# Performance work log

Hardware: AMD Instinct MI355X
Metric: run time of the kernel (lower is better)

## Reference

```python
import jax, jax.numpy as jnp
import numpy as np

N_HEAD = 8
NORM_GROUPS = 32
EPS = 1e-6


def setup_inputs() -> dict:
    key = jax.random.key(0)
    ks = jax.random.split(key, 9)
    B, C, H, W, D = 1, 256, 16, 16, 16
    COND = 512
    x = jax.random.normal(ks[0], (B, C, H, W, D), dtype=jnp.float32)
    cond = jax.random.normal(ks[1], (B, COND), dtype=jnp.float32)
    # AdaGN linear scale/shift (torch Linear: weight [C, cond_dim], bias [C])
    w_scale = jax.random.normal(ks[2], (C, COND), dtype=jnp.float32) * 0.02
    b_scale = jax.random.normal(ks[3], (C,), dtype=jnp.float32) * 0.02
    w_shift = jax.random.normal(ks[4], (C, COND), dtype=jnp.float32) * 0.02
    b_shift = jax.random.normal(ks[5], (C,), dtype=jnp.float32) * 0.02
    # 1x1x1 conv3d weights collapse to matrices: qkv [3C, C] (no bias), out [C, C] + bias
    w_qkv = jax.random.normal(ks[6], (3 * C, C), dtype=jnp.float32) * (1.0 / np.sqrt(C))
    w_out = jax.random.normal(ks[7], (C, C), dtype=jnp.float32) * (1.0 / np.sqrt(C))
    b_out = jax.random.normal(ks[8], (C,), dtype=jnp.float32) * 0.02
    return {"x": x, "cond": cond, "w_scale": w_scale, "b_scale": b_scale,
            "w_shift": w_shift, "b_shift": b_shift, "w_qkv": w_qkv,
            "w_out": w_out, "b_out": b_out}


def _ada_gn(x, cond, w_scale, b_scale, w_shift, b_shift):
    B, C, H, W, D = x.shape
    G = NORM_GROUPS
    xg = x.reshape(B, G, C // G, H, W, D)
    mean = jnp.mean(xg, axis=(2, 3, 4, 5), keepdims=True)
    var = jnp.var(xg, axis=(2, 3, 4, 5), keepdims=True)
    x_norm = ((xg - mean) * jax.lax.rsqrt(var + EPS)).reshape(B, C, H, W, D)
    scale = (cond @ w_scale.T + b_scale)[:, :, None, None, None]  # [B,C,1,1,1]
    shift = (cond @ w_shift.T + b_shift)[:, :, None, None, None]
    return x_norm * (1.0 + scale) + shift


def reference(x, cond, w_scale, b_scale, w_shift, b_shift, w_qkv, w_out, b_out):
    B, C, H, W, D = x.shape
    nh = N_HEAD
    hd = C // nh
    N = H * W * D  # flattened spatial tokens
    norm = _ada_gn(x, cond, w_scale, b_scale, w_shift, b_shift)
    # 1x1x1 conv == channel matmul
    qkv = jnp.einsum('oc,bchwd->bohwd', w_qkv, norm)        # [B,3C,H,W,D]
    qkv = qkv.reshape(B, nh, 3 * hd, N)
    q, k, v = jnp.split(qkv, 3, axis=2)                      # each [B,nh,hd,N]
    attn = jnp.einsum('bnci,bncj->bnij', q, k) / jnp.sqrt(jnp.float32(C))
    attn = jax.nn.softmax(attn, axis=-1)                     # [B,nh,N,N]
    out = jnp.einsum('bnij,bncj->bnci', attn, v)             # [B,nh,hd,N]
    out = out.reshape(B, C, H, W, D)
    out = jnp.einsum('oc,bchwd->bohwd', w_out, out) + b_out[None, :, None, None, None]
    return out + x
```

## Files before the change

kernel.cpp:

```cpp
#include <hip/hip_runtime.h>
#include <math.h>

#define CCH 256
#define NN  4096
#define NHEAD 8
#define CONDD 512

typedef __attribute__((ext_vector_type(8))) short short8;
typedef __attribute__((ext_vector_type(4))) float f32x4;
typedef __attribute__((ext_vector_type(16))) float f32x16;

static __device__ __forceinline__ short f2bf(float f) {
    union { float f; uint32_t u; } v; v.f = f;
    uint32_t r = v.u + 0x7fffu + ((v.u >> 16) & 1u);
    return (short)(r >> 16);
}

static __device__ __forceinline__ uint32_t cvt_pk_bf16(float a, float b) {
    uint32_t r;
    asm("v_cvt_pk_bf16_f32 %0, %1, %2" : "=v"(r) : "v"(a), "v"(b));
    return r;
}

__global__ __launch_bounds__(256) void front_fused(const float* __restrict__ x,
                                                   const float* __restrict__ cond,
                                                   const float* __restrict__ w_scale,
                                                   const float* __restrict__ b_scale,
                                                   const float* __restrict__ w_shift,
                                                   const float* __restrict__ b_shift,
                                                   const float* __restrict__ wq,
                                                   const float* __restrict__ wo,
                                                   float* __restrict__ partial,
                                                   float* __restrict__ scale,
                                                   float* __restrict__ shift,
                                                   short* __restrict__ wqb,
                                                   short* __restrict__ wob) {
    __shared__ float rs[4], rss[4];
    int bb = blockIdx.x;
    int t = threadIdx.x;
    if (bb < 256) {
        const float4* p = (const float4*)(x + bb * 4096);
        float s = 0.f, ss = 0.f;
        for (int k = t; k < 1024; k += 256) {
            float4 v = p[k];
            s += v.x + v.y + v.z + v.w;
            ss += v.x * v.x + v.y * v.y + v.z * v.z + v.w * v.w;
        }
        #pragma unroll
        for (int off = 32; off; off >>= 1) { s += __shfl_xor(s, off); ss += __shfl_xor(ss, off); }
        int wid = t >> 6;
        if ((t & 63) == 0) { rs[wid] = s; rss[wid] = ss; }
        __syncthreads();
        if (t == 0) {
            partial[2 * bb] = rs[0] + rs[1] + rs[2] + rs[3];
            partial[2 * bb + 1] = rss[0] + rss[1] + rss[2] + rss[3];
        }
    } else if (bb < 1280) {
        int idx = (bb - 256) * 256 + t;
        if (idx < 196608) wqb[idx] = f2bf(wq[idx]);
        else              wob[idx - 196608] = f2bf(wo[idx - 196608]);
    } else {
        int o = (bb - 1280) * 4 + (t >> 6);
        int lane = t & 63;
        float ds = 0.f, dh = 0.f;
        for (int k = lane; k < CONDD; k += 64) {
            float cv = cond[k];
            ds += cv * w_scale[o * CONDD + k];
            dh += cv * w_shift[o * CONDD + k];
        }
        #pragma unroll
        for (int off = 32; off; off >>= 1) { ds += __shfl_xor(ds, off); dh += __shfl_xor(dh, off); }
        if (lane == 0) { scale[o] = ds + b_scale[o]; shift[o] = dh + b_shift[o]; }
    }
}

__global__ __launch_bounds__(256) void normalize_t(const float* __restrict__ x,
                                                   const float* __restrict__ partial,
                                                   const float* __restrict__ scale,
                                                   const float* __restrict__ shift,
                                                   short* __restrict__ norm_t) {
    __shared__ float gm[8], gr[8];
    __shared__ float Aa[64], Bb[64];
    __shared__ short tile[32 * 66];
    int i0 = blockIdx.x * 32;
    int c0 = blockIdx.y * 64;
    int g0 = c0 >> 3;
    int t = threadIdx.x;
    if (t < 8) {
        float s = 0.f, ss = 0.f;
        #pragma unroll
        for (int ch = 0; ch < 8; ++ch) {
            s += partial[((g0 + t) * 8 + ch) * 2];
            ss += partial[((g0 + t) * 8 + ch) * 2 + 1];
        }
        float mean = s * (1.0f / 32768.0f);
        float var = ss * (1.0f / 32768.0f) - mean * mean;
        gm[t] = mean;
        gr[t] = rsqrtf(var + 1e-6f);
    }
    __syncthreads();
    if (t < 64) {
        int c = c0 + t;
        float a = gr[t >> 3] * (1.0f + scale[c]);
        Aa[t] = a;
        Bb[t] = shift[c] - gm[t >> 3] * a;
    }
    __syncthreads();
    #pragma unroll
    for (int e0 = 0; e0 < 8; ++e0) {
        int e = e0 * 256 + t;
        int cl = e >> 5, il = e & 31;
        float v = x[(c0 + cl) * NN + i0 + il];
        tile[il * 66 + cl] = f2bf(v * Aa[cl] + Bb[cl]);
    }
    __syncthreads();
    #pragma unroll
    for (int e0 = 0; e0 < 4; ++e0) {
        int e = e0 * 256 + t;
        int il = e >> 5, cd = e & 31;
        uint32_t d = *(const uint32_t*)&tile[il * 66 + 2 * cd];
        *(uint32_t*)&norm_t[(i0 + il) * 256 + c0 + 2 * cd] = d;
    }
}

__global__ __launch_bounds__(256) void qkv_gemm(const short* __restrict__ wqb,
                                                const short* __restrict__ norm_t,
                                                short* __restrict__ qtb, short* __restrict__ ktb,
                                                short* __restrict__ vcb) {
    int t = threadIdx.x;
    int w = t >> 6, lane = t & 63, li = lane & 15, lg = lane >> 4;
    int o0 = blockIdx.x * 32;
    int i0 = blockIdx.y * 64 + w * 16;
    f32x4 acc[2] = {{0,0,0,0},{0,0,0,0}};
    const short* bbase = norm_t + (i0 + li) * 256 + 8 * lg;
    const short* abase = wqb + (o0 + li) * 256 + 8 * lg;
    #pragma unroll
    for (int ks = 0; ks < 8; ++ks) {
        short8 bfrag = *(const short8*)(bbase + ks * 32);
        #pragma unroll
        for (int f = 0; f < 2; ++f) {
            short8 afrag = *(const short8*)(abase + f * 16 * 256 + ks * 32);
            acc[f] = __builtin_amdgcn_mfma_f32_16x16x32_bf16(afrag, bfrag, acc[f], 0, 0, 0);
        }
    }
    int i = i0 + li;
    #pragma unroll
    for (int f = 0; f < 2; ++f) {
        #pragma unroll
        for (int r = 0; r < 4; ++r) {
            int o = o0 + 16 * f + 4 * lg + r;
            float v = acc[f][r];
            int h = o / 96;
            int rr = o - h * 96;
            int cc = rr & 31;
            int kind = rr >> 5;
            if (kind == 0)      qtb[(h * NN + i) * 32 + cc] = f2bf(v * (0.0625f * 1.44269504f));
            else if (kind == 1) ktb[(h * NN + i) * 32 + cc] = f2bf(v);
            else                vcb[(h * 32 + cc) * NN + i] = f2bf(v);
        }
    }
}

__global__ __launch_bounds__(256, 4) void attention_mfma(const short* __restrict__ qtb,
                                                         const short* __restrict__ ktb,
                                                         const short* __restrict__ vcb,
                                                         float* __restrict__ pacc,
                                                         float* __restrict__ plsum) {
    __shared__ __align__(16) short kbuf[2][2048];
    __shared__ __align__(16) short vbuf[2][2048];

    int bid = blockIdx.x;
    int h = bid & 7;
    int qb = (bid >> 3) & 31;
    int kh = bid >> 8;
    int t = threadIdx.x;
    int w = t >> 6, lane = t & 63, l31 = lane & 31, hi = lane >> 5;

    int qbase = qb * 128 + w * 32;
    const short* qrow = qtb + (h * NN + qbase + l31) * 32;
    short8 qf0 = *(const short8*)(qrow + 8 * hi);
    short8 qf1 = *(const short8*)(qrow + 16 + 8 * hi);

    int kr_ = t >> 2, ks_ = t & 3, kg_ = ks_ ^ (kr_ & 3);
    int vr_ = t >> 3, vs_ = t & 7, vg_ = vs_ ^ (vr_ & 7);
    const char* kgbase = (const char*)(ktb + (h * NN + kh * 2048) * 32) + kr_ * 64 + kg_ * 16;
    const char* vgbase = (const char*)(vcb + (h * 32 + vr_) * NN + kh * 2048) + vg_ * 16;
    int wave_off = (t >> 6) * 1024;

    f32x16 acc = {0,0,0,0,0,0,0,0,0,0,0,0,0,0,0,0};
    const f32x16 zero16 = {0,0,0,0,0,0,0,0,0,0,0,0,0,0,0,0};
    float lsum = 0.f;

    __builtin_amdgcn_global_load_lds((const uint32_t*)kgbase, (uint32_t*)((char*)&kbuf[0][0] + wave_off), 16, 0, 0);
    __builtin_amdgcn_global_load_lds((const uint32_t*)vgbase, (uint32_t*)((char*)&vbuf[0][0] + wave_off), 16, 0, 0);
    __syncthreads();

    #pragma unroll 1
    for (int st = 0; st < 32; ++st) {
        int cur = st & 1;
        if (st < 31) {
            const char* kn = kgbase + (st + 1) * 4096;
            const char* vn = vgbase + (st + 1) * 128;
            __builtin_amdgcn_global_load_lds((const uint32_t*)kn, (uint32_t*)((char*)&kbuf[cur ^ 1][0] + wave_off), 16, 0, 0);
            __builtin_amdgcn_global_load_lds((const uint32_t*)vn, (uint32_t*)((char*)&vbuf[cur ^ 1][0] + wave_off), 16, 0, 0);
        }

        #pragma unroll
        for (int half = 0; half < 2; ++half) {
            int jl = half * 32;
            int R = jl + l31;
            const short* kr = &kbuf[cur][R * 32];
            int rx = R & 3;
            short8 kf0 = *(const short8*)(kr + ((hi ^ rx) << 3));
            short8 kf1 = *(const short8*)(kr + (((2 + hi) ^ rx) << 3));
            const short* vr = &vbuf[cur][l31 * 64];
            int cx = l31 & 7;
            int s0 = (jl >> 3) + hi;
            short8 vf0 = *(const short8*)(vr + ((s0 ^ cx) << 3));
            short8 vf1 = *(const short8*)(vr + (((s0 + 2) ^ cx) << 3));

            __builtin_amdgcn_s_setprio(1);
            f32x16 s = __builtin_amdgcn_mfma_f32_32x32x16_bf16(kf0, qf0, zero16, 0, 0, 0);
            s = __builtin_amdgcn_mfma_f32_32x32x16_bf16(kf1, qf1, s, 0, 0, 0);
            __builtin_amdgcn_s_setprio(0);

            float p[16];
            #pragma unroll
            for (int r = 0; r < 16; ++r) p[r] = __builtin_amdgcn_exp2f(s[r]);

            float u0 = 0.f, u1 = 0.f;
            #pragma unroll
            for (int r = 0; r < 4; ++r) { u0 += p[r] + p[4 + r]; u1 += p[8 + r] + p[12 + r]; }
            lsum += u0 + u1;

            auto A1 = __builtin_amdgcn_permlane32_swap(cvt_pk_bf16(p[0], p[1]),   cvt_pk_bf16(p[4], p[5]),   false, false);
            auto A2 = __builtin_amdgcn_permlane32_swap(cvt_pk_bf16(p[2], p[3]),   cvt_pk_bf16(p[6], p[7]),   false, false);
            auto A3 = __builtin_amdgcn_permlane32_swap(cvt_pk_bf16(p[8], p[9]),   cvt_pk_bf16(p[12], p[13]), false, false);
            auto A4 = __builtin_amdgcn_permlane32_swap(cvt_pk_bf16(p[10], p[11]), cvt_pk_bf16(p[14], p[15]), false, false);

            union PF { uint32_t u[4]; short8 s8; };
            PF f1, f2;
            f1.u[0] = A1[0]; f1.u[1] = A2[0]; f1.u[2] = A1[1]; f1.u[3] = A2[1];
            f2.u[0] = A3[0]; f2.u[1] = A4[0]; f2.u[2] = A3[1]; f2.u[3] = A4[1];

            __builtin_amdgcn_s_setprio(1);
            acc = __builtin_amdgcn_mfma_f32_32x32x16_bf16(vf0, f1.s8, acc, 0, 0, 0);
            acc = __builtin_amdgcn_mfma_f32_32x32x16_bf16(vf1, f2.s8, acc, 0, 0, 0);
            __builtin_amdgcn_s_setprio(0);
        }
        __syncthreads();
    }

    lsum += __shfl_xor(lsum, 32);

    int qg = qbase + l31;
    float* pb = pacc + ((kh * 8 + h) * 32) * NN + qg;
    #pragma unroll
    for (int r = 0; r < 16; ++r) {
        int c = (r & 3) + 8 * (r >> 2) + 4 * hi;
        pb[c * NN] = acc[r];
    }
    if (hi == 0) plsum[(kh * 8 + h) * NN + qg] = lsum;
}

__global__ __launch_bounds__(256) void attn_merge(const float* __restrict__ pacc,
                                                  const float* __restrict__ plsum,
                                                  short* __restrict__ attnT) {
    __shared__ float tile[64][33];
    __shared__ float invl[64];
    int it = blockIdx.x;
    int h = blockIdx.y;
    int t = threadIdx.x;
    int i0 = it * 64;
    int c = t >> 3, ic = (t & 7) * 8;
    const float* p0 = pacc + (h * 32 + c) * NN + i0 + ic;
    const float* p1 = pacc + ((8 + h) * 32 + c) * NN + i0 + ic;
    #pragma unroll
    for (int k = 0; k < 8; ++k) tile[ic + k][c] = p0[k] + p1[k];
    if (t < 64) {
        float ls = plsum[h * NN + i0 + t] + plsum[(8 + h) * NN + i0 + t];
        invl[t] = 1.0f / ls;
    }
    __syncthreads();
    int i = t >> 2, cs = (t & 3) * 8;
    float iv = invl[i];
    const float* tr = &tile[i][cs];
    uint4 o;
    o.x = cvt_pk_bf16(tr[0] * iv, tr[1] * iv);
    o.y = cvt_pk_bf16(tr[2] * iv, tr[3] * iv);
    o.z = cvt_pk_bf16(tr[4] * iv, tr[5] * iv);
    o.w = cvt_pk_bf16(tr[6] * iv, tr[7] * iv);
    *(uint4*)&attnT[(i0 + i) * 256 + h * 32 + cs] = o;
}

__global__ __launch_bounds__(256) void proj_gemm(const short* __restrict__ wob,
                                                 const short* __restrict__ attnT,
                                                 const float* __restrict__ b_out,
                                                 const float* __restrict__ x,
                                                 float* __restrict__ out) {
    int t = threadIdx.x;
    int w = t >> 6, lane = t & 63, li = lane & 15, lg = lane >> 4;
    int o0 = blockIdx.x * 32;
    int i0 = blockIdx.y * 64 + w * 16;
    f32x4 acc[2] = {{0,0,0,0},{0,0,0,0}};
    const short* bbase = attnT + (i0 + li) * 256 + 8 * lg;
    const short* abase = wob + (o0 + li) * 256 + 8 * lg;
    #pragma unroll
    for (int ks = 0; ks < 8; ++ks) {
        short8 bfrag = *(const short8*)(bbase + ks * 32);
        #pragma unroll
        for (int f = 0; f < 2; ++f) {
            short8 afrag = *(const short8*)(abase + f * 16 * 256 + ks * 32);
            acc[f] = __builtin_amdgcn_mfma_f32_16x16x32_bf16(afrag, bfrag, acc[f], 0, 0, 0);
        }
    }
    int i = i0 + li;
    #pragma unroll
    for (int f = 0; f < 2; ++f) {
        #pragma unroll
        for (int r = 0; r < 4; ++r) {
            int o = o0 + 16 * f + 4 * lg + r;
            out[o * NN + i] = acc[f][r] + b_out[o] + x[o * NN + i];
        }
    }
}

extern "C" void kernel_launch(void* const* d_in, const int* in_sizes, int n_in,
                              void* d_out, int out_size, void* d_ws, size_t ws_size,
                              hipStream_t stream) {
    const float* x       = (const float*)d_in[0];
    const float* cond    = (const float*)d_in[1];
    const float* w_scale = (const float*)d_in[2];
    const float* b_scale = (const float*)d_in[3];
    const float* w_shift = (const float*)d_in[4];
    const float* b_shift = (const float*)d_in[5];
    const float* w_qkv   = (const float*)d_in[6];
    const float* w_out   = (const float*)d_in[7];
    const float* b_out   = (const float*)d_in[8];
    float* out = (float*)d_out;

    float* ws = (float*)d_ws;
    float* scale   = ws;
    float* shift   = ws + 256;
    float* partial = ws + 512;
    short* norm_t = (short*)(ws + 1024);
    short* qtb = norm_t + 1048576;
    short* ktb = qtb + 1048576;
    short* vcb = ktb + 1048576;
    short* attnT = vcb + 1048576;
    short* wqb = attnT + 1048576;
    short* wob = wqb + 768 * 256;
    float* pacc  = (float*)(wob + 65536);
    float* plsum = pacc + 2 * 8 * 32 * NN;

    front_fused<<<1344, 256, 0, stream>>>(x, cond, w_scale, b_scale, w_shift, b_shift,
                                          w_qkv, w_out, partial, scale, shift, wqb, wob);
    normalize_t<<<dim3(128, 4), 256, 0, stream>>>(x, partial, scale, shift, norm_t);
    qkv_gemm<<<dim3(24, 64), 256, 0, stream>>>(wqb, norm_t, qtb, ktb, vcb);
    attention_mfma<<<512, 256, 0, stream>>>(qtb, ktb, vcb, pacc, plsum);
    attn_merge<<<dim3(64, 8), 256, 0, stream>>>(pacc, plsum, attnT);
    proj_gemm<<<dim3(8, 64), 256, 0, stream>>>(wob, attnT, b_out, x, out);
}
```

Baseline: 76.64 us.

## Split attention keys four ways and double the per-stage tile size

The attention kernel now splits the key dimension into four partitions instead of two, launching 1024 blocks so more work is spread across the GPU's compute units. Each pipeline stage loads two 64-key chunks at once, which halves the number of barrier-separated stages while doubling LDS use per block. The merge kernel sums four partial accumulators and row-sums instead of two. In exchange this adds extra global traffic for the partial results and doubles LDS per block, which may lower occupancy.

```diff
diff --git a/kernel.cpp b/kernel.cpp
--- a/kernel.cpp
+++ b/kernel.cpp
@@ -166,8 +166,8 @@
                                                          const short* __restrict__ vcb,
                                                          float* __restrict__ pacc,
                                                          float* __restrict__ plsum) {
-    __shared__ __align__(16) short kbuf[2][2048];
-    __shared__ __align__(16) short vbuf[2][2048];
+    __shared__ __align__(16) short kbuf[2][2][2048];
+    __shared__ __align__(16) short vbuf[2][2][2048];
 
     int bid = blockIdx.x;
     int h = bid & 7;
@@ -183,70 +183,77 @@
 
     int kr_ = t >> 2, ks_ = t & 3, kg_ = ks_ ^ (kr_ & 3);
     int vr_ = t >> 3, vs_ = t & 7, vg_ = vs_ ^ (vr_ & 7);
-    const char* kgbase = (const char*)(ktb + (h * NN + kh * 2048) * 32) + kr_ * 64 + kg_ * 16;
-    const char* vgbase = (const char*)(vcb + (h * 32 + vr_) * NN + kh * 2048) + vg_ * 16;
-    int wave_off = (t >> 6) * 1024;
+    const char* kgbase = (const char*)(ktb + (h * NN + kh * 1024) * 32) + kr_ * 64 + kg_ * 16;
+    const char* vgbase = (const char*)(vcb + (h * 32 + vr_) * NN + kh * 1024) + vg_ * 16;
+    int wave_off = w * 1024;
 
     f32x16 acc = {0,0,0,0,0,0,0,0,0,0,0,0,0,0,0,0};
     const f32x16 zero16 = {0,0,0,0,0,0,0,0,0,0,0,0,0,0,0,0};
     float lsum = 0.f;
 
-    __builtin_amdgcn_global_load_lds((const uint32_t*)kgbase, (uint32_t*)((char*)&kbuf[0][0] + wave_off), 16, 0, 0);
-    __builtin_amdgcn_global_load_lds((const uint32_t*)vgbase, (uint32_t*)((char*)&vbuf[0][0] + wave_off), 16, 0, 0);
+    __builtin_amdgcn_global_load_lds((const uint32_t*)(kgbase),        (uint32_t*)((char*)&kbuf[0][0][0] + wave_off), 16, 0, 0);
+    __builtin_amdgcn_global_load_lds((const uint32_t*)(kgbase + 4096), (uint32_t*)((char*)&kbuf[0][1][0] + wave_off), 16, 0, 0);
+    __builtin_amdgcn_global_load_lds((const uint32_t*)(vgbase),        (uint32_t*)((char*)&vbuf[0][0][0] + wave_off), 16, 0, 0);
+    __builtin_amdgcn_global_load_lds((const uint32_t*)(vgbase + 128),  (uint32_t*)((char*)&vbuf[0][1][0] + wave_off), 16, 0, 0);
     __syncthreads();
 
     #pragma unroll 1
-    for (int st = 0; st < 32; ++st) {
+    for (int st = 0; st < 8; ++st) {
         int cur = st & 1;
-        if (st < 31) {
-            const char* kn = kgbase + (st + 1) * 4096;
-            const char* vn = vgbase + (st + 1) * 128;
-            __builtin_amdgcn_global_load_lds((const uint32_t*)kn, (uint32_t*)((char*)&kbuf[cur ^ 1][0] + wave_off), 16, 0, 0);
-            __builtin_amdgcn_global_load_lds((const uint32_t*)vn, (uint32_t*)((char*)&vbuf[cur ^ 1][0] + wave_off), 16, 0, 0);
-        }
-
-        #pragma unroll
-        for (int half = 0; half < 2; ++half) {
-            int jl = half * 32;
-            int R = jl + l31;
-            const short* kr = &kbuf[cur][R * 32];
-            int rx = R & 3;
-            short8 kf0 = *(const short8*)(kr + ((hi ^ rx) << 3));
-            short8 kf1 = *(const short8*)(kr + (((2 + hi) ^ rx) << 3));
-            const short* vr = &vbuf[cur][l31 * 64];
-            int cx = l31 & 7;
-            int s0 = (jl >> 3) + hi;
-            short8 vf0 = *(const short8*)(vr + ((s0 ^ cx) << 3));
-            short8 vf1 = *(const short8*)(vr + (((s0 + 2) ^ cx) << 3));
-
-            __builtin_amdgcn_s_setprio(1);
-            f32x16 s = __builtin_amdgcn_mfma_f32_32x32x16_bf16(kf0, qf0, zero16, 0, 0, 0);
-            s = __builtin_amdgcn_mfma_f32_32x32x16_bf16(kf1, qf1, s, 0, 0, 0);
-            __builtin_amdgcn_s_setprio(0);
-
-            float p[16];
+        if (st < 7) {
+            const char* kn = kgbase + (st + 1) * 8192;
+            const char* vn = vgbase + (st + 1) * 256;
+            __builtin_amdgcn_global_load_lds((const uint32_t*)(kn),        (uint32_t*)((char*)&kbuf[cur ^ 1][0][0] + wave_off), 16, 0, 0);
+            __builtin_amdgcn_global_load_lds((const uint32_t*)(kn + 4096), (uint32_t*)((char*)&kbuf[cur ^ 1][1][0] + wave_off), 16, 0, 0);
+            __builtin_amdgcn_global_load_lds((const uint32_t*)(vn),        (uint32_t*)((char*)&vbuf[cur ^ 1][0][0] + wave_off), 16, 0, 0);
+            __builtin_amdgcn_global_load_lds((const uint32_t*)(vn + 128),  (uint32_t*)((char*)&vbuf[cur ^ 1][1][0] + wave_off), 16, 0, 0);
+        }
+
+        #pragma unroll
+        for (int chunk = 0; chunk < 2; ++chunk) {
             #pragma unroll
-            for (int r = 0; r < 16; ++r) p[r] = __builtin_amdgcn_exp2f(s[r]);
-
-            float u0 = 0.f, u1 = 0.f;
-            #pragma unroll
-            for (int r = 0; r < 4; ++r) { u0 += p[r] + p[4 + r]; u1 += p[8 + r] + p[12 + r]; }
-            lsum += u0 + u1;
-
-            auto A1 = __builtin_amdgcn_permlane32_swap(cvt_pk_bf16(p[0], p[1]),   cvt_pk_bf16(p[4], p[5]),   false, false);
-            auto A2 = __builtin_amdgcn_permlane32_swap(cvt_pk_bf16(p[2], p[3]),   cvt_pk_bf16(p[6], p[7]),   false, false);
-            auto A3 = __builtin_amdgcn_permlane32_swap(cvt_pk_bf16(p[8], p[9]),   cvt_pk_bf16(p[12], p[13]), false, false);
-            auto A4 = __builtin_amdgcn_permlane32_swap(cvt_pk_bf16(p[10], p[11]), cvt_pk_bf16(p[14], p[15]), false, false);
-
-            union PF { uint32_t u[4]; short8 s8; };
-            PF f1, f2;
-            f1.u[0] = A1[0]; f1.u[1] = A2[0]; f1.u[2] = A1[1]; f1.u[3] = A2[1];
-            f2.u[0] = A3[0]; f2.u[1] = A4[0]; f2.u[2] = A3[1]; f2.u[3] = A4[1];
-
-            __builtin_amdgcn_s_setprio(1);
-            acc = __builtin_amdgcn_mfma_f32_32x32x16_bf16(vf0, f1.s8, acc, 0, 0, 0);
-            acc = __builtin_amdgcn_mfma_f32_32x32x16_bf16(vf1, f2.s8, acc, 0, 0, 0);
-            __builtin_amdgcn_s_setprio(0);
+            for (int half = 0; half < 2; ++half) {
+                int jl = half * 32;
+                int R = jl + l31;
+                const short* kr = &kbuf[cur][chunk][R * 32];
+                int rx = R & 3;
+                short8 kf0 = *(const short8*)(kr + ((hi ^ rx) << 3));
+                short8 kf1 = *(const short8*)(kr + (((2 + hi) ^ rx) << 3));
+                const short* vr = &vbuf[cur][chunk][l31 * 64];
+                int cx = l31 & 7;
+                int s0 = (jl >> 3) + hi;
+                short8 vf0 = *(const short8*)(vr + ((s0 ^ cx) << 3));
+                short8 vf1 = *(const short8*)(vr + (((s0 + 2) ^ cx) << 3));
+
+                __builtin_amdgcn_s_setprio(1);
+                f32x16 s = __builtin_amdgcn_mfma_f32_32x32x16_bf16(kf0, qf0, zero16, 0, 0, 0);
+                s = __builtin_amdgcn_mfma_f32_32x32x16_bf16(kf1, qf1, s, 0, 0, 0);
+                __builtin_amdgcn_s_setprio(0);
+
+                float p[16];
+                #pragma unroll
+                for (int r = 0; r < 16; ++r) p[r] = __builtin_amdgcn_exp2f(s[r]);
+
+                float u0 = 0.f, u1 = 0.f;
+                #pragma unroll
+                for (int r = 0; r < 4; ++r) { u0 += p[r] + p[4 + r]; u1 += p[8 + r] + p[12 + r]; }
+                lsum += u0 + u1;
+
+                auto A1 = __builtin_amdgcn_permlane32_swap(cvt_pk_bf16(p[0], p[1]),   cvt_pk_bf16(p[4], p[5]),   false, false);
+                auto A2 = __builtin_amdgcn_permlane32_swap(cvt_pk_bf16(p[2], p[3]),   cvt_pk_bf16(p[6], p[7]),   false, false);
+                auto A3 = __builtin_amdgcn_permlane32_swap(cvt_pk_bf16(p[8], p[9]),   cvt_pk_bf16(p[12], p[13]), false, false);
+                auto A4 = __builtin_amdgcn_permlane32_swap(cvt_pk_bf16(p[10], p[11]), cvt_pk_bf16(p[14], p[15]), false, false);
+
+                union PF { uint32_t u[4]; short8 s8; };
+                PF f1, f2;
+                f1.u[0] = A1[0]; f1.u[1] = A2[0]; f1.u[2] = A1[1]; f1.u[3] = A2[1];
+                f2.u[0] = A3[0]; f2.u[1] = A4[0]; f2.u[2] = A3[1]; f2.u[3] = A4[1];
+
+                __builtin_amdgcn_s_setprio(1);
+                acc = __builtin_amdgcn_mfma_f32_32x32x16_bf16(vf0, f1.s8, acc, 0, 0, 0);
+                acc = __builtin_amdgcn_mfma_f32_32x32x16_bf16(vf1, f2.s8, acc, 0, 0, 0);
+                __builtin_amdgcn_s_setprio(0);
+            }
         }
         __syncthreads();
     }
@@ -274,11 +281,17 @@
     int i0 = it * 64;
     int c = t >> 3, ic = (t & 7) * 8;
     const float* p0 = pacc + (h * 32 + c) * NN + i0 + ic;
-    const float* p1 = pacc + ((8 + h) * 32 + c) * NN + i0 + ic;
-    #pragma unroll
-    for (int k = 0; k < 8; ++k) tile[ic + k][c] = p0[k] + p1[k];
+    #pragma unroll
+    for (int k = 0; k < 8; ++k) {
+        float s = 0.f;
+        #pragma unroll
+        for (int q4 = 0; q4 < 4; ++q4) s += p0[q4 * 8 * 32 * NN + k];
+        tile[ic + k][c] = s;
+    }
     if (t < 64) {
-        float ls = plsum[h * NN + i0 + t] + plsum[(8 + h) * NN + i0 + t];
+        float ls = 0.f;
+        #pragma unroll
+        for (int q4 = 0; q4 < 4; ++q4) ls += plsum[(q4 * 8 + h) * NN + i0 + t];
         invl[t] = 1.0f / ls;
     }
     __syncthreads();
@@ -351,13 +364,13 @@
     short* wqb = attnT + 1048576;
     short* wob = wqb + 768 * 256;
     float* pacc  = (float*)(wob + 65536);
-    float* plsum = pacc + 2 * 8 * 32 * NN;
+    float* plsum = pacc + 4 * 8 * 32 * NN;
 
     front_fused<<<1344, 256, 0, stream>>>(x, cond, w_scale, b_scale, w_shift, b_shift,
                                           w_qkv, w_out, partial, scale, shift, wqb, wob);
     normalize_t<<<dim3(128, 4), 256, 0, stream>>>(x, partial, scale, shift, norm_t);
     qkv_gemm<<<dim3(24, 64), 256, 0, stream>>>(wqb, norm_t, qtb, ktb, vcb);
-    attention_mfma<<<512, 256, 0, stream>>>(qtb, ktb, vcb, pacc, plsum);
+    attention_mfma<<<1024, 256, 0, stream>>>(qtb, ktb, vcb, pacc, plsum);
     attn_merge<<<dim3(64, 8), 256, 0, stream>>>(pacc, plsum, attnT);
     proj_gemm<<<dim3(8, 64), 256, 0, stream>>>(wob, attnT, b_out, x, out);
 }
```

After: 72.68 us. 5.2% less time.
